# Kernel optimization log

Measured on AMD Instinct MI355X. Metric: run time of the kernel, lower is better.

## Reference

```python
import math
import jax, jax.numpy as jnp
import numpy as np
from jax.scipy.special import gammaln, xlogy

B, N1, N2 = 4, 2048, 512
D, H, DK = 768, 8, 64
DV = D // H        # 96 (dim_value = dim // heads)
NRP = D // H       # 96 num_rel_pos_features (divisible by 6)
DY0 = 1280 + 256   # esm_dim + cell_line_dim
EPS = 1e-5
SCALE = DK ** -0.5


def layer_norm(z, g, b):
    m = jnp.mean(z, -1, keepdims=True)
    v = jnp.mean(jnp.square(z - m), -1, keepdims=True)
    return (z - m) * jax.lax.rsqrt(v + EPS) * g + b


def get_positional_embed(seq_len, feature_size):
    # Enformer-style relative positional features over distances [-(L-1), L-1]
    d = jnp.arange(-seq_len + 1, seq_len)
    ad = jnp.abs(d).astype(jnp.float32)[:, None]  # [2L-1, 1]
    nb = feature_size // 6
    # exponential half-life basis
    max_range = math.log(seq_len) / math.log(2.0)
    half_life = 2.0 ** jnp.linspace(3.0, max_range, nb)
    f_exp = jnp.exp(-math.log(2.0) / half_life * ad)
    # central mask basis
    cw = 2.0 ** jnp.arange(1, nb + 1).astype(jnp.float32) - 1.0
    f_cm = (cw > ad).astype(jnp.float32)
    # gamma pdf basis
    stddev = seq_len / (2.0 * nb)
    start_mean = seq_len / nb
    mean = jnp.linspace(start_mean, float(seq_len), nb)
    conc = (mean / stddev) ** 2
    rate = mean / (stddev ** 2)
    logp = xlogy(conc - 1.0, ad) - rate * ad - (gammaln(conc) - conc * jnp.log(rate))
    prob = jnp.exp(logp) + 1e-8
    f_g = prob / jnp.max(prob, -1, keepdims=True)
    emb = jnp.concatenate([f_exp, f_cm, f_g], -1)  # [2L-1, feature_size/2]
    sign = jnp.sign(d).astype(jnp.float32)[:, None]
    return jnp.concatenate([emb, sign * emb], -1)  # [2L-1, feature_size]


def relative_shift(z):
    # Transformer-XL shift: [b,h,i,2*L-1] -> [b,h,i,L]
    b, h, i, j = z.shape
    z = jnp.pad(z, ((0, 0), (0, 0), (0, 0), (1, 0)))
    z = z.reshape(b, h, j + 1, i)[:, :, 1:, :].reshape(b, h, i, j)
    return z[..., : (j + 2) // 2]


def ffn(z, g, b, w1, b1, w2, b2):
    h = layer_norm(z, g, b)
    h = jax.nn.relu(h @ w1 + b1)
    return z + h @ w2 + b2


def setup_inputs() -> dict:
    key = jax.random.key(0)
    ks = jax.random.split(key, 32)
    p = lambda i, shape, s=0.02: jax.random.normal(ks[i], shape, jnp.float32) * s
    return dict(
        x=jax.random.normal(ks[0], (B, N1, D), jnp.float32),
        y0=jax.random.normal(ks[1], (B, N2, DY0), jnp.float32),
        W_res=p(2, (DY0, D)),
        lnx_g=jnp.ones((D,)), lnx_b=jnp.zeros((D,)),
        lny_g=jnp.ones((D,)), lny_b=jnp.zeros((D,)),
        Wq=p(3, (D, H * DK)), Wk=p(4, (D, H * DK)),
        Wv1=p(5, (D, H * DV)), Wv2=p(6, (D, H * DV)),
        Wo1=p(7, (H * DV, D)), bo1=jnp.zeros((D,)),
        Wo2=p(8, (H * DV, D)), bo2=jnp.zeros((D,)),
        Wrel=p(9, (NRP, H * DK)),
        rel_pos_bias=p(10, (H, DK), 1.0),
        fx_g=jnp.ones((D,)), fx_b=jnp.zeros((D,)),
        fx_w1=p(11, (D, 2 * D)), fx_b1=jnp.zeros((2 * D,)),
        fx_w2=p(12, (2 * D, D)), fx_b2=jnp.zeros((D,)),
        fy_g=jnp.ones((D,)), fy_b=jnp.zeros((D,)),
        fy_w1=p(13, (D, 2 * D)), fy_b1=jnp.zeros((2 * D,)),
        fy_w2=p(14, (2 * D, D)), fy_b2=jnp.zeros((D,)),
    )


def reference(x, y0, W_res, lnx_g, lnx_b, lny_g, lny_b, Wq, Wk, Wv1, Wv2,
              Wo1, bo1, Wo2, bo2, Wrel, rel_pos_bias,
              fx_g, fx_b, fx_w1, fx_b1, fx_w2, fx_b2,
              fy_g, fy_b, fy_w1, fy_b1, fy_w2, fy_b2):
    b, n1, _ = x.shape
    n2 = y0.shape[1]
    y = y0 @ W_res                               # res_proj (first layer)
    x1 = layer_norm(x, lnx_g, lnx_b)
    y1 = layer_norm(y, lny_g, lny_b)

    q = (x1 @ Wq).reshape(b, n1, H, DK).transpose(0, 2, 1, 3) * SCALE
    k = (y1 @ Wk).reshape(b, n2, H, DK).transpose(0, 2, 1, 3)
    v2 = (y1 @ Wv2).reshape(b, n2, H, DV).transpose(0, 2, 1, 3)

    content = jnp.einsum('bhid,bhjd->bhij', q, k)  # [b,h,n1,n2]

    pos = get_positional_embed(n1, NRP)            # [2*n1-1, NRP]
    rel_q = (pos @ Wrel).reshape(2 * n1 - 1, H, DK).transpose(1, 0, 2)
    kb = k * SCALE + rel_pos_bias[None, :, None, :]
    rel = jnp.einsum('bhjd,hmd->bhjm', kb, rel_q)  # [b,h,n2,2*n1-1]
    rel = relative_shift(rel)                      # [b,h,n2,n1]
    logits = content + rel.transpose(0, 1, 3, 2)

    attn = jax.nn.softmax(logits, -1)
    out1 = jnp.einsum('bhij,bhjd->bhid', attn, v2)
    out1 = out1.transpose(0, 2, 1, 3).reshape(b, n1, H * DV)
    x2 = out1 @ Wo1 + bo1

    v1 = (x1 @ Wv1).reshape(b, n1, H, DV).transpose(0, 2, 1, 3)
    out2 = jnp.einsum('bhij,bhid->bhjd', attn, v1)  # attn^T @ v1
    out2 = out2.transpose(0, 2, 1, 3).reshape(b, n2, H * DV)
    y2 = out2 @ Wo2 + bo2

    x4 = x + x2
    x5 = ffn(x4, fx_g, fx_b, fx_w1, fx_b1, fx_w2, fx_b2)
    y4 = y2 + y
    y5 = ffn(y4, fy_g, fy_b, fy_w1, fy_b1, fy_w2, fy_b2)
    return (x5, y5)
```

## Files before the change

kernel.cpp:

```cpp
#include <hip/hip_runtime.h>
#include <hip/hip_bf16.h>
#include <math.h>

typedef __hip_bfloat16 bf16;
typedef short s16x8 __attribute__((ext_vector_type(8)));
typedef short s16x4 __attribute__((ext_vector_type(4)));
typedef float f32x4 __attribute__((ext_vector_type(4)));

#define B_    4
#define N1_   2048
#define N2_   512
#define D_    768
#define H_    8
#define DK_   64
#define DV_   96
#define NPOS_ 4095
#define SCALE_ 0.125f

__device__ __forceinline__ float b2f(bf16 v) { return __bfloat162float(v); }
__device__ __forceinline__ bf16  f2b(float v) { return __float2bfloat16(v); }
__device__ __forceinline__ float us2f(unsigned short u) {
    return __uint_as_float(((unsigned int)u) << 16);
}
__device__ __forceinline__ unsigned short f2bu(float v) {
    bf16 t = __float2bfloat16(v);
    return *reinterpret_cast<unsigned short*>(&t);
}
__device__ __forceinline__ float ldf(const float* p) { return *p; }
__device__ __forceinline__ float ldf(const bf16* p)  { return __bfloat162float(*p); }
__device__ __forceinline__ void stf(float* p, float v) { *p = v; }
__device__ __forceinline__ void stf(bf16* p, float v)  { *p = f2b(v); }
#define MFMA16(a, b, c) __builtin_amdgcn_mfma_f32_16x16x32_bf16((a), (b), (c), 0, 0, 0)

__device__ __forceinline__ void gl16(const unsigned short* g, unsigned short* l) {
    __builtin_amdgcn_global_load_lds(
        (const __attribute__((address_space(1))) unsigned int*)g,
        (__attribute__((address_space(3))) unsigned int*)l, 16, 0, 0);
}

struct PackT {
    const float* src[12];
    unsigned K[12], N[12], dbase[12], drow[12];
    unsigned t0[13];
};

__global__ __launch_bounds__(256) void packT_kernel(PackT pa, bf16* __restrict__ dst)
{
    int bid = blockIdx.x, s = 0;
    while (s < 11 && bid >= (int)pa.t0[s + 1]) s++;
    int t = bid - (int)pa.t0[s];
    unsigned K = pa.K[s], N = pa.N[s];
    unsigned ntk = K >> 5;
    unsigned k0 = (t % ntk) << 5, n0 = (t / ntk) << 6;
    __shared__ float tile[32][65];
    const float* src = pa.src[s];
    int tid = threadIdx.x;
    {
        int e = tid * 8, k = e >> 6, n = e & 63;
        const float* p = src + (size_t)(k0 + k) * N + n0 + n;
#pragma unroll
        for (int j = 0; j < 8; j++) tile[k][n + j] = p[j];
    }
    __syncthreads();
    {
        int f = tid * 8, n = f >> 5, k = f & 31;
        bf16* q = dst + (size_t)pa.dbase[s] + (size_t)(n0 + n) * pa.drow[s] + k0 + k;
#pragma unroll
        for (int j = 0; j < 8; j++) q[j] = f2b(tile[k + j][n]);
    }
}

template <typename T>
__global__ __launch_bounds__(64) void lnfull_kernel(
    const T* __restrict__ in, const float* __restrict__ g,
    const float* __restrict__ b, bf16* __restrict__ out)
{
    int row = blockIdx.x, lane = threadIdx.x;
    const T* p = in + (size_t)row * D_;
    float v[12];
    float s = 0.f;
#pragma unroll
    for (int i = 0; i < 12; i++) { v[i] = ldf(p + lane + i * 64); s += v[i]; }
#pragma unroll
    for (int o = 32; o > 0; o >>= 1) s += __shfl_down(s, o);
    float mean = __shfl(s, 0) * (1.f / 768.f);
    float var = 0.f;
#pragma unroll
    for (int i = 0; i < 12; i++) { float d = v[i] - mean; var += d * d; }
#pragma unroll
    for (int o = 32; o > 0; o >>= 1) var += __shfl_down(var, o);
    float rstd = rsqrtf(__shfl(var, 0) * (1.f / 768.f) + 1e-5f);
    bf16* q = out + (size_t)row * D_;
#pragma unroll
    for (int i = 0; i < 12; i++) {
        int c = lane + i * 64;
        q[c] = f2b((v[i] - mean) * rstd * g[c] + b[c]);
    }
}

template <int AM, typename TC, typename TR>
__device__ __forceinline__ void gemm128_body(
    unsigned short* As, unsigned short* Bs, int tid,
    const void* Av, const bf16* BwT, TC* C, int M, int N, int K,
    const float* bias, int relu, const TR* res,
    bf16* Cq, bf16* Cv, bf16* Cq2, const float* qbias2,
    float sscale, int vshift, int bm, int bn)
{
    int wave = tid >> 6, lane = tid & 63;
    int lc = lane & 15, kq = lane >> 4;
    int wm = (wave & 1) * 64, wn = (wave >> 1) * 64;
    f32x4 acc[4][4] = {};
    int grow = tid >> 3, gcol = (tid & 7) * 8;
    const unsigned short* bg = (const unsigned short*)BwT + (size_t)(bn + grow) * K + gcol;
    unsigned short* asl = As + wave * 512;
    unsigned short* bsl = Bs + wave * 512;
    const size_t SL = (size_t)B_ * N2_ * 768;

    for (int k0 = 0; k0 < K; k0 += 64) {
        if (AM == 0) {
            const unsigned short* ag = (const unsigned short*)Av + (size_t)(bm + grow) * K + k0 + gcol;
#pragma unroll
            for (int it = 0; it < 4; it++)
                gl16(ag + (size_t)(it * 32) * K, asl + it * 2048);
        } else {
#pragma unroll
            for (int it = 0; it < 4; it++) {
                const unsigned short* a0 = (const unsigned short*)Av
                    + (size_t)(bm + grow + it * 32) * K + k0 + gcol;
                s16x8 v0 = *reinterpret_cast<const s16x8*>(a0);
                s16x8 v1 = *reinterpret_cast<const s16x8*>(a0 + SL);
                s16x8 v2 = *reinterpret_cast<const s16x8*>(a0 + 2 * SL);
                s16x8 v3 = *reinterpret_cast<const s16x8*>(a0 + 3 * SL);
                s16x8 w;
#pragma unroll
                for (int j = 0; j < 8; j++)
                    w[j] = (short)f2bu(us2f((unsigned short)v0[j]) + us2f((unsigned short)v1[j]) +
                                       us2f((unsigned short)v2[j]) + us2f((unsigned short)v3[j]));
                *reinterpret_cast<s16x8*>(&As[(grow + it * 32) * 64 + gcol]) = w;
            }
        }
#pragma unroll
        for (int it = 0; it < 4; it++)
            gl16(bg + (size_t)(it * 32) * K + k0, bsl + it * 2048);
        __syncthreads();
#pragma unroll
        for (int kh = 0; kh < 2; kh++) {
            s16x8 af[4], bf[4];
#pragma unroll
            for (int mt = 0; mt < 4; mt++)
                af[mt] = *reinterpret_cast<const s16x8*>(&As[(wm + mt * 16 + lc) * 64 + kh * 32 + kq * 8]);
#pragma unroll
            for (int nt = 0; nt < 4; nt++)
                bf[nt] = *reinterpret_cast<const s16x8*>(&Bs[(wn + nt * 16 + lc) * 64 + kh * 32 + kq * 8]);
#pragma unroll
            for (int mt = 0; mt < 4; mt++)
#pragma unroll
                for (int nt = 0; nt < 4; nt++)
                    acc[mt][nt] = MFMA16(af[mt], bf[nt], acc[mt][nt]);
        }
        __syncthreads();
    }

#pragma unroll
    for (int mt = 0; mt < 4; mt++) {
#pragma unroll
        for (int nt = 0; nt < 4; nt++) {
            int n = bn + wn + nt * 16 + lc;
            float bv = (!Cq && bias) ? bias[n] : 0.f;
#pragma unroll
            for (int r = 0; r < 4; r++) {
                int m = bm + wm + mt * 16 + kq * 4 + r;
                float vr = acc[mt][nt][r];
                if (Cq) {
                    int rows = 1 << vshift;
                    int bb = m >> vshift, rr = m & (rows - 1);
                    if (n < 512) {
                        size_t off = (((size_t)bb * 8 + (n >> 6)) * rows + rr) * 64 + (n & 63);
                        Cq[off] = f2b(vr * sscale);
                        if (Cq2) Cq2[off] = f2b(vr * SCALE_ + qbias2[n]);
                    } else {
                        int nn = n - 512, hh = nn / 96, dv = nn - hh * 96;
                        Cv[(((size_t)bb * 8 + hh) * rows + rr) * 96 + dv] = f2b(vr);
                    }
                } else {
                    float v = vr + bv;
                    if (relu) v = fmaxf(v, 0.f);
                    size_t off = (size_t)m * N + n;
                    if (res) v += ldf(res + off);
                    stf(C + off, v);
                }
            }
        }
    }
}

struct GP {
    const void* Av; const bf16* BwT; void* C;
    int M, N, K;
    const float* bias; int relu; const void* res;
    bf16 *Cq, *Cv, *Cq2; const float* qbias2;
    float sscale; int vshift; int nbx, nwg;
};

template <int AMA, int AMB, typename TC, typename TR>
__global__ __launch_bounds__(256, 4) void dual128_kernel(GP a, GP b)
{
    __shared__ __align__(16) unsigned short As[128 * 64];
    __shared__ __align__(16) unsigned short Bs[128 * 64];
    int tid = threadIdx.x;
    int bid = blockIdx.x;
    if (bid < a.nwg) {
        int sbid = (a.nwg & 7) ? bid : ((bid & 7) * (a.nwg >> 3) + (bid >> 3));
        gemm128_body<AMA, TC, TR>(As, Bs, tid, a.Av, a.BwT, (TC*)a.C,
            a.M, a.N, a.K, a.bias, a.relu, (const TR*)a.res,
            a.Cq, a.Cv, a.Cq2, a.qbias2, a.sscale, a.vshift,
            (sbid / a.nbx) * 128, (sbid % a.nbx) * 128);
    } else {
        int lb = bid - a.nwg;
        int sbid = (b.nwg & 7) ? lb : ((lb & 7) * (b.nwg >> 3) + (lb >> 3));
        gemm128_body<AMB, TC, TR>(As, Bs, tid, b.Av, b.BwT, (TC*)b.C,
            b.M, b.N, b.K, b.bias, b.relu, (const TR*)b.res,
            b.Cq, b.Cv, b.Cq2, b.qbias2, b.sscale, b.vshift,
            (sbid / b.nbx) * 128, (sbid % b.nbx) * 128);
    }
}

template <int AM, typename TC>
__global__ __launch_bounds__(256) void mgemm64_kernel(
    const void* __restrict__ Av, const bf16* __restrict__ BwT,
    TC* __restrict__ C, int M, int N, int K)
{
    __shared__ unsigned short As[64][40];
    __shared__ unsigned short Bs[64][40];
    int tid = threadIdx.x, wave = tid >> 6, lane = tid & 63;
    int bm = blockIdx.y * 64, bn = blockIdx.x * 64;
    f32x4 acc[4] = {};
    int am = tid >> 2, ak = (tid & 3) * 8;
    int bn_ = tid & 63, bk = (tid >> 6) * 8;
    const unsigned short* bwt = (const unsigned short*)BwT;

    for (int k0 = 0; k0 < K; k0 += 32) {
        if (AM == 0) {
            s16x8 va = {};
            if (bm + am < M)
                va = *reinterpret_cast<const s16x8*>(
                    (const unsigned short*)Av + (size_t)(bm + am) * K + k0 + ak);
            *reinterpret_cast<s16x8*>(&As[am][ak]) = va;
        } else {
            const float* ap = (const float*)Av + (size_t)(bm + am) * K + k0 + ak;
#pragma unroll
            for (int j = 0; j < 8; j++)
                As[am][ak + j] = (bm + am < M) ? f2bu(ap[j]) : (unsigned short)0;
        }
        *reinterpret_cast<s16x8*>(&Bs[bn_][bk]) =
            *reinterpret_cast<const s16x8*>(bwt + (size_t)(bn + bn_) * K + k0 + bk);
        __syncthreads();

        s16x8 afrag = *reinterpret_cast<const s16x8*>(&As[wave * 16 + (lane & 15)][(lane >> 4) * 8]);
#pragma unroll
        for (int ns = 0; ns < 4; ns++) {
            s16x8 bfrag = *reinterpret_cast<const s16x8*>(&Bs[ns * 16 + (lane & 15)][(lane >> 4) * 8]);
            acc[ns] = MFMA16(afrag, bfrag, acc[ns]);
        }
        __syncthreads();
    }

    int col = lane & 15, rg = (lane >> 4) * 4;
#pragma unroll
    for (int ns = 0; ns < 4; ns++) {
        int n = bn + ns * 16 + col;
#pragma unroll
        for (int r = 0; r < 4; r++) {
            int m = bm + wave * 16 + rg + r;
            if (m >= M) continue;
            stf(C + (size_t)m * N + n, acc[ns][r]);
        }
    }
}

__global__ __launch_bounds__(64) void pos_kernel(bf16* __restrict__ pos)
{
    int m = blockIdx.x * 64 + threadIdx.x;
    if (m >= NPOS_) return;
    float dist = (float)(m - 2047);
    float ad = fabsf(dist);
    float sgn = (dist > 0.f) ? 1.f : ((dist < 0.f) ? -1.f : 0.f);
    float f[48];
#pragma unroll
    for (int t = 0; t < 16; t++) {
        float hl = exp2f(3.f + (8.f / 15.f) * (float)t);
        f[t] = expf(-0.69314718056f / hl * ad);
    }
#pragma unroll
    for (int t = 0; t < 16; t++) {
        float cw = exp2f((float)(t + 1)) - 1.f;
        f[16 + t] = (cw > ad) ? 1.f : 0.f;
    }
    float pr[16];
    float mx = 0.f;
    if (ad < 0.5f) {
#pragma unroll
        for (int t = 0; t < 16; t++) pr[t] = 1e-8f;
        mx = 1e-8f;
    } else {
        float lad = logf(ad);
#pragma unroll
        for (int t = 0; t < 16; t++) {
            float mean = 128.f * (float)(t + 1);
            float cc = (mean / 64.f) * (mean / 64.f);
            float rate = mean * (1.f / 4096.f);
            float logp = (cc - 1.f) * lad - rate * ad - (lgammaf(cc) - cc * logf(rate));
            float p = expf(logp) + 1e-8f;
            pr[t] = p;
            mx = fmaxf(mx, p);
        }
    }
#pragma unroll
    for (int t = 0; t < 16; t++) f[32 + t] = pr[t] / mx;

    bf16* o = pos + (size_t)m * 96;
#pragma unroll
    for (int c = 0; c < 48; c++) { o[c] = f2b(f[c]); o[48 + c] = f2b(sgn * f[c]); }
}

#define TP_ 344
__global__ __launch_bounds__(256) void tshift_kernel(
    const bf16* __restrict__ kbb, const bf16* __restrict__ relq,
    bf16* __restrict__ tsh, int base, int plen)
{
    int mc = blockIdx.x, jt = blockIdx.y, bh = blockIdx.z;
    int mbase = mc << 8, jg0 = jt << 6, h = bh & 7;
    int iwin0 = mbase + jg0 - 511 - base;
    if (iwin0 + 318 < 0 || iwin0 >= plen) return;
    int a0 = iwin0 & 7;
    int iwa = iwin0 - a0;
    __shared__ unsigned short Tl[64][TP_];
    int tid = threadIdx.x, wave = tid >> 6, lane = tid & 63;
    int lc = lane & 15, kq = lane >> 4;

    const bf16* ap = kbb + ((size_t)bh * N2_ + jg0 + wave * 16 + lc) * 64 + kq * 8;
    s16x8 af0 = *reinterpret_cast<const s16x8*>(ap);
    s16x8 af1 = *reinterpret_cast<const s16x8*>(ap + 32);

    int jrow = wave * 16 + kq * 4;
#pragma unroll
    for (int sub = 0; sub < 2; sub++) {
        int m0 = mbase + sub * 128;
        f32x4 tacc[8] = {};
#pragma unroll
        for (int ns = 0; ns < 8; ns++) {
            const bf16* rp = relq + (size_t)(m0 + ns * 16 + lc) * 512 + h * 64 + kq * 8;
            s16x8 rf0 = *reinterpret_cast<const s16x8*>(rp);
            s16x8 rf1 = *reinterpret_cast<const s16x8*>(rp + 32);
            tacc[ns] = MFMA16(af0, rf0, tacc[ns]);
            tacc[ns] = MFMA16(af1, rf1, tacc[ns]);
        }
#pragma unroll
        for (int ns = 0; ns < 8; ns++)
#pragma unroll
            for (int r = 0; r < 4; r++) {
                int col = sub * 128 + ns * 16 + lc + jrow + r + a0;
                Tl[jrow + r][col] = f2bu(tacc[ns][r]);
            }
    }
    __syncthreads();

    int row = tid >> 2, q = tid & 3;
    int cstart = row + a0;
    bf16* out = tsh + ((size_t)bh * N2_ + jg0 + row) * (size_t)plen;
#pragma unroll
    for (int s = 0; s < 11; s++) {
        int c = (q + s * 4) * 8;
        int i = iwa + c;
        if (c >= cstart && c + 8 <= cstart + 256 && i >= 0 && i + 8 <= plen) {
            *reinterpret_cast<s16x8*>(out + i) =
                *reinterpret_cast<const s16x8*>(&Tl[row][c]);
        } else {
#pragma unroll
            for (int e = 0; e < 8; e++) {
                int ce = c + e, ie = i + e;
                if (ce >= cstart && ce < cstart + 256 && ie >= 0 && ie < plen)
                    out[ie] = *reinterpret_cast<const bf16*>(&Tl[row][ce]);
            }
        }
    }
}

__global__ __launch_bounds__(256) void attn1_kernel(
    const bf16* __restrict__ qb, const bf16* __restrict__ kb,
    const bf16* __restrict__ tsh, const bf16* __restrict__ v2,
    bf16* __restrict__ out1, float* __restrict__ mst, float* __restrict__ lst,
    int base, int tpitch)
{
    int bh = blockIdx.y;
    int b = bh >> 3, h = bh & 7;
    int i0 = base + blockIdx.x * 64;
    __shared__ __align__(16) unsigned short Ts[64][72];
    __shared__ __align__(16) unsigned short Ps[64][72];
    __shared__ __align__(16) unsigned short Vs[96][72];
    int tid = threadIdx.x, wave = tid >> 6, lane = tid & 63;
    int lc = lane & 15, kq = lane >> 4;
    int ibase = wave * 16 + kq * 4;

    const bf16* qp = qb + ((size_t)bh * N1_ + i0 + wave * 16 + lc) * 64 + kq * 8;
    s16x8 qf0 = *reinterpret_cast<const s16x8*>(qp);
    s16x8 qf1 = *reinterpret_cast<const s16x8*>(qp + 32);

    int trow = tid >> 2, tchunk = tid & 3;
    const unsigned short* tb0 = (const unsigned short*)tsh
        + ((size_t)bh * N2_ + trow) * tpitch + (i0 - base) + tchunk * 16;
    const unsigned short* vb0 = (const unsigned short*)v2
        + ((size_t)bh * N2_ + trow) * 96 + tchunk * 24;

    float m_run[4], l_run[4];
#pragma unroll
    for (int r = 0; r < 4; r++) { m_run[r] = -1e30f; l_run[r] = 0.f; }
    f32x4 oacc[6] = {};

    for (int j0 = 0; j0 < N2_; j0 += 64) {
        __syncthreads();
        {
            const unsigned short* p = tb0 + (size_t)j0 * tpitch;
            *reinterpret_cast<s16x8*>(&Ts[trow][tchunk * 16]) =
                *reinterpret_cast<const s16x8*>(p);
            *reinterpret_cast<s16x8*>(&Ts[trow][tchunk * 16 + 8]) =
                *reinterpret_cast<const s16x8*>(p + 8);
        }
        {
            const unsigned short* p = vb0 + (size_t)j0 * 96;
            s16x8 w0 = *reinterpret_cast<const s16x8*>(p);
            s16x8 w1 = *reinterpret_cast<const s16x8*>(p + 8);
            s16x8 w2 = *reinterpret_cast<const s16x8*>(p + 16);
            int vd = tchunk * 24;
#pragma unroll
            for (int s = 0; s < 8; s++) Vs[vd + s][trow] = (unsigned short)w0[s];
#pragma unroll
            for (int s = 0; s < 8; s++) Vs[vd + 8 + s][trow] = (unsigned short)w1[s];
#pragma unroll
            for (int s = 0; s < 8; s++) Vs[vd + 16 + s][trow] = (unsigned short)w2[s];
        }
        __syncthreads();

        f32x4 cacc[4] = {};
#pragma unroll
        for (int ns = 0; ns < 4; ns++) {
            const bf16* kp = kb + ((size_t)bh * N2_ + j0 + ns * 16 + lc) * 64 + kq * 8;
            s16x8 kf0 = *reinterpret_cast<const s16x8*>(kp);
            s16x8 kf1 = *reinterpret_cast<const s16x8*>(kp + 32);
            cacc[ns] = MFMA16(qf0, kf0, cacc[ns]);
            cacc[ns] = MFMA16(qf1, kf1, cacc[ns]);
        }
        float Lv[4][4];
#pragma unroll
        for (int ns = 0; ns < 4; ns++) {
            int jloc = ns * 16 + lc;
            s16x4 tv = *reinterpret_cast<const s16x4*>(&Ts[jloc][ibase]);
#pragma unroll
            for (int r = 0; r < 4; r++)
                Lv[ns][r] = cacc[ns][r] + us2f((unsigned short)tv[r]);
        }
#pragma unroll
        for (int r = 0; r < 4; r++) {
            float v = fmaxf(fmaxf(Lv[0][r], Lv[1][r]), fmaxf(Lv[2][r], Lv[3][r]));
            v = fmaxf(v, __shfl_xor(v, 1));
            v = fmaxf(v, __shfl_xor(v, 2));
            v = fmaxf(v, __shfl_xor(v, 4));
            v = fmaxf(v, __shfl_xor(v, 8));
            float mn = fmaxf(m_run[r], v);
            float alpha = __expf(m_run[r] - mn);
            m_run[r] = mn;
            float s = 0.f;
#pragma unroll
            for (int ns = 0; ns < 4; ns++) {
                float p = __expf(Lv[ns][r] - mn);
                Lv[ns][r] = p;
                s += p;
            }
            s += __shfl_xor(s, 1);
            s += __shfl_xor(s, 2);
            s += __shfl_xor(s, 4);
            s += __shfl_xor(s, 8);
            l_run[r] = l_run[r] * alpha + s;
#pragma unroll
            for (int ns6 = 0; ns6 < 6; ns6++) oacc[ns6][r] *= alpha;
        }
#pragma unroll
        for (int ns = 0; ns < 4; ns++)
#pragma unroll
            for (int r = 0; r < 4; r++)
                Ps[ibase + r][ns * 16 + lc] = f2bu(Lv[ns][r]);
#pragma unroll
        for (int kk = 0; kk < 2; kk++) {
            s16x8 pf = *reinterpret_cast<const s16x8*>(&Ps[wave * 16 + lc][kq * 8 + kk * 32]);
#pragma unroll
            for (int ns6 = 0; ns6 < 6; ns6++) {
                s16x8 vf = *reinterpret_cast<const s16x8*>(&Vs[ns6 * 16 + lc][kq * 8 + kk * 32]);
                oacc[ns6] = MFMA16(pf, vf, oacc[ns6]);
            }
        }
    }

    float invl[4];
#pragma unroll
    for (int r = 0; r < 4; r++) invl[r] = 1.f / l_run[r];
#pragma unroll
    for (int ns6 = 0; ns6 < 6; ns6++)
#pragma unroll
        for (int r = 0; r < 4; r++)
            out1[(size_t)(b * N1_ + i0 + ibase + r) * 768 + h * 96 + ns6 * 16 + lc]
                = f2b(oacc[ns6][r] * invl[r]);
    if (lc == 0) {
#pragma unroll
        for (int r = 0; r < 4; r++) {
            mst[(size_t)bh * N1_ + i0 + ibase + r] = m_run[r];
            lst[(size_t)bh * N1_ + i0 + ibase + r] = l_run[r];
        }
    }
}

__global__ __launch_bounds__(256) void attn2_kernel(
    const bf16* __restrict__ qb, const bf16* __restrict__ kb,
    const bf16* __restrict__ tsh, const bf16* __restrict__ v1,
    bf16* __restrict__ out2b, const float* __restrict__ mst,
    const float* __restrict__ lst, int base, int tpitch)
{
    int jt = blockIdx.x, bh = blockIdx.y;
    int b = bh >> 3, h = bh & 7;
    int ib = base + blockIdx.z * 512;
    bf16* out2 = out2b + (size_t)(ib >> 9) * ((size_t)B_ * N2_ * 768);
    int j0 = jt * 64;
    __shared__ __align__(16) unsigned short Ts[64][72];
    __shared__ __align__(16) unsigned short Ps[64][72];
    __shared__ __align__(16) unsigned short Vs[96][72];
    int tid = threadIdx.x, wave = tid >> 6, lane = tid & 63;
    int lc = lane & 15, kq = lane >> 4;
    int ibase = wave * 16 + kq * 4;

    s16x8 kf0[4], kf1[4];
#pragma unroll
    for (int ns = 0; ns < 4; ns++) {
        const bf16* kp = kb + ((size_t)bh * N2_ + j0 + ns * 16 + lc) * 64 + kq * 8;
        kf0[ns] = *reinterpret_cast<const s16x8*>(kp);
        kf1[ns] = *reinterpret_cast<const s16x8*>(kp + 32);
    }

    int trow = tid >> 2, tchunk = tid & 3;
    const unsigned short* tb0 = (const unsigned short*)tsh
        + ((size_t)bh * N2_ + j0 + trow) * tpitch + tchunk * 16;
    const unsigned short* vb0 = (const unsigned short*)v1
        + ((size_t)bh * N1_ + trow) * 96 + tchunk * 24;

    f32x4 oacc[6] = {};
    for (int i0 = ib; i0 < ib + 512; i0 += 64) {
        __syncthreads();
        {
            const unsigned short* p = tb0 + (i0 - base);
            *reinterpret_cast<s16x8*>(&Ts[trow][tchunk * 16]) =
                *reinterpret_cast<const s16x8*>(p);
            *reinterpret_cast<s16x8*>(&Ts[trow][tchunk * 16 + 8]) =
                *reinterpret_cast<const s16x8*>(p + 8);
        }
        {
            const unsigned short* p = vb0 + (size_t)i0 * 96;
            s16x8 w0 = *reinterpret_cast<const s16x8*>(p);
            s16x8 w1 = *reinterpret_cast<const s16x8*>(p + 8);
            s16x8 w2 = *reinterpret_cast<const s16x8*>(p + 16);
            int vd = tchunk * 24;
#pragma unroll
            for (int s = 0; s < 8; s++) Vs[vd + s][trow] = (unsigned short)w0[s];
#pragma unroll
            for (int s = 0; s < 8; s++) Vs[vd + 8 + s][trow] = (unsigned short)w1[s];
#pragma unroll
            for (int s = 0; s < 8; s++) Vs[vd + 16 + s][trow] = (unsigned short)w2[s];
        }
        __syncthreads();

        const bf16* qp = qb + ((size_t)bh * N1_ + i0 + wave * 16 + lc) * 64 + kq * 8;
        s16x8 qf0 = *reinterpret_cast<const s16x8*>(qp);
        s16x8 qf1 = *reinterpret_cast<const s16x8*>(qp + 32);
        f32x4 cacc[4] = {};
#pragma unroll
        for (int ns = 0; ns < 4; ns++) {
            cacc[ns] = MFMA16(qf0, kf0[ns], cacc[ns]);
            cacc[ns] = MFMA16(qf1, kf1[ns], cacc[ns]);
        }
        float mi[4], invli[4];
#pragma unroll
        for (int r = 0; r < 4; r++) {
            mi[r] = mst[(size_t)bh * N1_ + i0 + ibase + r];
            invli[r] = 1.f / lst[(size_t)bh * N1_ + i0 + ibase + r];
        }
#pragma unroll
        for (int ns = 0; ns < 4; ns++) {
            int jloc = ns * 16 + lc;
            s16x4 tv = *reinterpret_cast<const s16x4*>(&Ts[jloc][ibase]);
            s16x4 pw;
#pragma unroll
            for (int r = 0; r < 4; r++) {
                float L = cacc[ns][r] + us2f((unsigned short)tv[r]);
                pw[r] = (short)f2bu(__expf(L - mi[r]) * invli[r]);
            }
            *reinterpret_cast<s16x4*>(&Ps[jloc][ibase]) = pw;
        }
        __syncthreads();
#pragma unroll
        for (int kk = 0; kk < 2; kk++) {
            s16x8 pf = *reinterpret_cast<const s16x8*>(&Ps[wave * 16 + lc][kq * 8 + kk * 32]);
#pragma unroll
            for (int ns6 = 0; ns6 < 6; ns6++) {
                s16x8 vf = *reinterpret_cast<const s16x8*>(&Vs[ns6 * 16 + lc][kq * 8 + kk * 32]);
                oacc[ns6] = MFMA16(pf, vf, oacc[ns6]);
            }
        }
    }

#pragma unroll
    for (int ns6 = 0; ns6 < 6; ns6++)
#pragma unroll
        for (int r = 0; r < 4; r++)
            out2[(size_t)(b * N2_ + j0 + ibase + r) * 768 + h * 96 + ns6 * 16 + lc]
                = f2b(oacc[ns6][r]);
}

extern "C" void kernel_launch(void* const* d_in, const int* in_sizes, int n_in,
                              void* d_out, int out_size, void* d_ws, size_t ws_size,
                              hipStream_t stream)
{
    (void)in_sizes; (void)n_in; (void)out_size;
    const float* x      = (const float*)d_in[0];
    const float* y0     = (const float*)d_in[1];
    const float* Wres   = (const float*)d_in[2];
    const float* lnx_g  = (const float*)d_in[3];
    const float* lnx_b  = (const float*)d_in[4];
    const float* lny_g  = (const float*)d_in[5];
    const float* lny_b  = (const float*)d_in[6];
    const float* Wq     = (const float*)d_in[7];
    const float* Wk     = (const float*)d_in[8];
    const float* Wv1    = (const float*)d_in[9];
    const float* Wv2    = (const float*)d_in[10];
    const float* Wo1    = (const float*)d_in[11];
    const float* bo1    = (const float*)d_in[12];
    const float* Wo2    = (const float*)d_in[13];
    const float* bo2    = (const float*)d_in[14];
    const float* Wrel   = (const float*)d_in[15];
    const float* rel_pb = (const float*)d_in[16];
    const float* fx_g   = (const float*)d_in[17];
    const float* fx_b   = (const float*)d_in[18];
    const float* fx_w1  = (const float*)d_in[19];
    const float* fx_b1  = (const float*)d_in[20];
    const float* fx_w2  = (const float*)d_in[21];
    const float* fx_b2  = (const float*)d_in[22];
    const float* fy_g   = (const float*)d_in[23];
    const float* fy_b   = (const float*)d_in[24];
    const float* fy_w1  = (const float*)d_in[25];
    const float* fy_b1  = (const float*)d_in[26];
    const float* fy_w2  = (const float*)d_in[27];
    const float* fy_b2  = (const float*)d_in[28];

    float* out_x = (float*)d_out;
    float* out_y = out_x + (size_t)B_ * N1_ * D_;
    bf16* out1 = (bf16*)d_out;

    char* W = (char*)d_ws;
    size_t o = 0;
    auto alloc = [&](size_t bytes) { char* p = W + o; o += (bytes + 255) & ~(size_t)255; return p; };
    bf16*   qb   = (bf16*)alloc((size_t)B_ * N1_ * 512 * 2);
    bf16*   kb   = (bf16*)alloc((size_t)B_ * N2_ * 512 * 2);
    bf16*   posb = (bf16*)alloc((size_t)NPOS_ * 96 * 2);
    bf16*   relq = (bf16*)alloc((size_t)NPOS_ * 512 * 2);
    bf16*   v1b  = (bf16*)alloc((size_t)B_ * N1_ * 768 * 2);
    bf16*   hx2  = (bf16*)alloc((size_t)B_ * N1_ * 768 * 2);
    bf16*   v2b  = (bf16*)alloc((size_t)B_ * N2_ * 768 * 2);
    float*  yb   = (float*)alloc((size_t)B_ * N2_ * 768 * 4);
    bf16*   kbbb = (bf16*)alloc((size_t)B_ * N2_ * 512 * 2);
    bf16*   wpool= (bf16*)alloc((size_t)9093120 * 2);
    float*  mst  = (float*)alloc((size_t)B_ * H_ * N1_ * 4);
    float*  lst  = (float*)alloc((size_t)B_ * H_ * N1_ * 4);

    size_t x1y1 = ((size_t)B_ * N1_ * 768 + (size_t)B_ * N2_ * 768) * 2;
    size_t rem = ws_size > o ? ws_size - o : 0;
    int plen = 512;
    if (rem >= (size_t)32 * 512 * 2048 * 2 + 1024) plen = 2048;
    else if (rem >= (size_t)32 * 512 * 1024 * 2 + 1024) plen = 1024;
    size_t tshB = (size_t)32 * 512 * (size_t)plen * 2;
    bf16* tshb = (bf16*)alloc(tshB > x1y1 ? tshB : x1y1);
    bf16* x1 = tshb;
    bf16* y1 = x1 + (size_t)B_ * N1_ * 768;

    bf16* x4 = qb;
    bf16* y4 = v2b;
    bf16* hx = v1b;
    bf16* out2h = hx2;
    bf16* hy = (bf16*)yb;
    bf16* x4ln = x1;
    bf16* y4ln = y1;

    const unsigned OW_RES = 0, OW_QV1 = 1179648, OW_KV2 = 2162688, OW_O1 = 3145728,
                   OW_O2 = 3735552, OW_REL = 4325376, OW_FXW1 = 4374528,
                   OW_FXW2 = 5554176, OW_FYW1 = 6733824, OW_FYW2 = 7913472;

    PackT pa;
    const float* srcs[12] = {Wres, Wq, Wv1, Wk, Wv2, Wo1, Wo2, Wrel,
                             fx_w1, fx_w2, fy_w1, fy_w2};
    unsigned Ks[12] = {1536, 768, 768, 768, 768, 768, 768, 96, 768, 1536, 768, 1536};
    unsigned Nss[12] = {768, 512, 768, 512, 768, 768, 768, 512, 1536, 768, 1536, 768};
    unsigned dbs[12] = {OW_RES, OW_QV1, OW_QV1 + 393216, OW_KV2, OW_KV2 + 393216,
                        OW_O1, OW_O2, OW_REL, OW_FXW1, OW_FXW2, OW_FYW1, OW_FYW2};
    unsigned drs[12] = {1536, 768, 768, 768, 768, 768, 768, 96, 768, 1536, 768, 1536};
    unsigned cum = 0;
    for (int i = 0; i < 12; i++) {
        pa.src[i] = srcs[i]; pa.K[i] = Ks[i]; pa.N[i] = Nss[i];
        pa.dbase[i] = dbs[i]; pa.drow[i] = drs[i];
        pa.t0[i] = cum;
        cum += (Ks[i] >> 5) * (Nss[i] >> 6);
    }
    pa.t0[12] = cum;

    dim3 blk(256);
    packT_kernel<<<cum, blk, 0, stream>>>(pa, wpool);
    mgemm64_kernel<1, float><<<dim3(12, 32), blk, 0, stream>>>(
        y0, wpool + OW_RES, yb, B_ * N2_, D_, 1536);
    lnfull_kernel<float><<<B_ * N1_, 64, 0, stream>>>(x, lnx_g, lnx_b, x1);
    lnfull_kernel<float><<<B_ * N2_, 64, 0, stream>>>(yb, lny_g, lny_b, y1);
    {
        GP a{x1, wpool + OW_QV1, nullptr, B_ * N1_, 1280, D_,
             nullptr, 0, nullptr, qb, v1b, nullptr, nullptr, SCALE_, 11, 10, 640};
        GP b{y1, wpool + OW_KV2, nullptr, B_ * N2_, 1280, D_,
             nullptr, 0, nullptr, kb, v2b, kbbb, rel_pb, 1.f, 9, 10, 160};
        dual128_kernel<0, 0, bf16, float><<<800, blk, 0, stream>>>(a, b);
    }
    pos_kernel<<<(NPOS_ + 63) / 64, 64, 0, stream>>>(posb);
    mgemm64_kernel<0, bf16><<<dim3(8, 64), blk, 0, stream>>>(
        posb, wpool + OW_REL, relq, NPOS_, 512, 96);
    for (int base = 0; base < N1_; base += plen) {
        tshift_kernel<<<dim3(10, 8, 32), blk, 0, stream>>>(kbbb, relq, tshb, base, plen);
        attn1_kernel<<<dim3(plen / 64, 32), blk, 0, stream>>>(
            qb, kb, tshb, v2b, out1, mst, lst, base, plen);
        attn2_kernel<<<dim3(8, 32, plen / 512), blk, 0, stream>>>(
            qb, kb, tshb, v1b, out2h, mst, lst, base, plen);
    }
    {
        GP a{out1, wpool + OW_O1, x4, B_ * N1_, D_, D_,
             bo1, 0, x, nullptr, nullptr, nullptr, nullptr, 0.f, 0, 6, 384};
        GP b{out2h, wpool + OW_O2, y4, B_ * N2_, D_, D_,
             bo2, 0, yb, nullptr, nullptr, nullptr, nullptr, 0.f, 0, 6, 96};
        dual128_kernel<0, 2, bf16, float><<<480, blk, 0, stream>>>(a, b);
    }
    lnfull_kernel<bf16><<<B_ * N1_, 64, 0, stream>>>(x4, fx_g, fx_b, x4ln);
    lnfull_kernel<bf16><<<B_ * N2_, 64, 0, stream>>>(y4, fy_g, fy_b, y4ln);
    {
        GP a{x4ln, wpool + OW_FXW1, hx, B_ * N1_, 1536, D_,
             fx_b1, 1, nullptr, nullptr, nullptr, nullptr, nullptr, 0.f, 0, 12, 768};
        GP b{y4ln, wpool + OW_FYW1, hy, B_ * N2_, 1536, D_,
             fy_b1, 1, nullptr, nullptr, nullptr, nullptr, nullptr, 0.f, 0, 12, 192};
        dual128_kernel<0, 0, bf16, float><<<960, blk, 0, stream>>>(a, b);
    }
    {
        GP a{hx, wpool + OW_FXW2, out_x, B_ * N1_, D_, 1536,
             fx_b2, 0, x4, nullptr, nullptr, nullptr, nullptr, 0.f, 0, 6, 384};
        GP b{hy, wpool + OW_FYW2, out_y, B_ * N2_, D_, 1536,
             fy_b2, 0, y4, nullptr, nullptr, nullptr, nullptr, 0.f, 0, 6, 96};
        dual128_kernel<0, 0, float, bf16><<<480, blk, 0, stream>>>(a, b);
    }
}
```

Baseline: 600.4 us.

## Split-K the y0 residual GEMM and fold rel-pos GEMM into QKV launch

The fp32-input 64x64 residual GEMM on y0 is replaced by an fp32-to-bf16 conversion pass, a 4-way split-K 128x128 MFMA GEMM writing partials, and a fused reduce+LayerNorm kernel that produces both yb and y1. The small pos@Wrel GEMM is appended as extra workgroups to the dual QKV GEMM launch, so it no longer needs its own launch. This targets low parallelism and slow per-element conversion in the old small-tile kernel, and also removes launch gaps. The cost is extra global traffic for the partial sums and the converted copy.

```diff
diff --git a/kernel.cpp b/kernel.cpp
--- a/kernel.cpp
+++ b/kernel.cpp
@@ -70,6 +70,21 @@
     }
 }
 
+__global__ __launch_bounds__(256) void cvt8_kernel(
+    const float* __restrict__ in, bf16* __restrict__ out)
+{
+    int i = (blockIdx.x * 256 + threadIdx.x) * 8;
+    f32x4 a = *reinterpret_cast<const f32x4*>(in + i);
+    f32x4 b = *reinterpret_cast<const f32x4*>(in + i + 4);
+    s16x8 w;
+#pragma unroll
+    for (int j = 0; j < 4; j++) {
+        w[j] = (short)f2bu(a[j]);
+        w[4 + j] = (short)f2bu(b[j]);
+    }
+    *reinterpret_cast<s16x8*>((unsigned short*)out + i) = w;
+}
+
 template <typename T>
 __global__ __launch_bounds__(64) void lnfull_kernel(
     const T* __restrict__ in, const float* __restrict__ g,
@@ -91,6 +106,101 @@
     for (int o = 32; o > 0; o >>= 1) var += __shfl_down(var, o);
     float rstd = rsqrtf(__shfl(var, 0) * (1.f / 768.f) + 1e-5f);
     bf16* q = out + (size_t)row * D_;
+#pragma unroll
+    for (int i = 0; i < 12; i++) {
+        int c = lane + i * 64;
+        q[c] = f2b((v[i] - mean) * rstd * g[c] + b[c]);
+    }
+}
+
+__global__ __launch_bounds__(256, 4) void wres_splitk_kernel(
+    const bf16* __restrict__ Av, const bf16* __restrict__ BwT,
+    float* __restrict__ Cp)
+{
+    __shared__ __align__(16) unsigned short As[128 * 64];
+    __shared__ __align__(16) unsigned short Bs[128 * 64];
+    const int K = 1536;
+    int tid = threadIdx.x, wave = tid >> 6, lane = tid & 63;
+    int lc = lane & 15, kq = lane >> 4;
+    int wm = (wave & 1) * 64, wn = (wave >> 1) * 64;
+    int bid = blockIdx.x;
+    int sbid = (bid & 7) * 48 + (bid >> 3);
+    int s = sbid / 96, t = sbid % 96;
+    int bm = (t / 6) * 128, bn = (t % 6) * 128;
+    int ks = s * 384;
+    f32x4 acc[4][4] = {};
+    int grow = tid >> 3, gcol = (tid & 7) * 8;
+    const unsigned short* ag = (const unsigned short*)Av + (size_t)(bm + grow) * K + gcol;
+    const unsigned short* bg = (const unsigned short*)BwT + (size_t)(bn + grow) * K + gcol;
+    unsigned short* asl = As + wave * 512;
+    unsigned short* bsl = Bs + wave * 512;
+
+    for (int k0 = ks; k0 < ks + 384; k0 += 64) {
+#pragma unroll
+        for (int it = 0; it < 4; it++) {
+            gl16(ag + (size_t)(it * 32) * K + k0, asl + it * 2048);
+            gl16(bg + (size_t)(it * 32) * K + k0, bsl + it * 2048);
+        }
+        __syncthreads();
+#pragma unroll
+        for (int kh = 0; kh < 2; kh++) {
+            s16x8 af[4], bf[4];
+#pragma unroll
+            for (int mt = 0; mt < 4; mt++)
+                af[mt] = *reinterpret_cast<const s16x8*>(&As[(wm + mt * 16 + lc) * 64 + kh * 32 + kq * 8]);
+#pragma unroll
+            for (int nt = 0; nt < 4; nt++)
+                bf[nt] = *reinterpret_cast<const s16x8*>(&Bs[(wn + nt * 16 + lc) * 64 + kh * 32 + kq * 8]);
+#pragma unroll
+            for (int mt = 0; mt < 4; mt++)
+#pragma unroll
+                for (int nt = 0; nt < 4; nt++)
+                    acc[mt][nt] = MFMA16(af[mt], bf[nt], acc[mt][nt]);
+        }
+        __syncthreads();
+    }
+
+    float* out = Cp + (size_t)s * (2048 * 768);
+#pragma unroll
+    for (int mt = 0; mt < 4; mt++)
+#pragma unroll
+        for (int nt = 0; nt < 4; nt++) {
+            int n = bn + wn + nt * 16 + lc;
+#pragma unroll
+            for (int r = 0; r < 4; r++) {
+                int m = bm + wm + mt * 16 + kq * 4 + r;
+                out[(size_t)m * 768 + n] = acc[mt][nt][r];
+            }
+        }
+}
+
+__global__ __launch_bounds__(64) void lnred4_kernel(
+    const float* __restrict__ Cp, const float* __restrict__ g,
+    const float* __restrict__ b, float* __restrict__ yb, bf16* __restrict__ y1)
+{
+    int row = blockIdx.x, lane = threadIdx.x;
+    const size_t SL = (size_t)2048 * 768;
+    const float* p = Cp + (size_t)row * 768;
+    float* yo = yb + (size_t)row * 768;
+    float v[12];
+    float s = 0.f;
+#pragma unroll
+    for (int i = 0; i < 12; i++) {
+        int c = lane + i * 64;
+        float t = p[c] + p[SL + c] + p[2 * SL + c] + p[3 * SL + c];
+        v[i] = t; s += t;
+        yo[c] = t;
+    }
+#pragma unroll
+    for (int o = 32; o > 0; o >>= 1) s += __shfl_down(s, o);
+    float mean = __shfl(s, 0) * (1.f / 768.f);
+    float var = 0.f;
+#pragma unroll
+    for (int i = 0; i < 12; i++) { float d = v[i] - mean; var += d * d; }
+#pragma unroll
+    for (int o = 32; o > 0; o >>= 1) var += __shfl_down(var, o);
+    float rstd = rsqrtf(__shfl(var, 0) * (1.f / 768.f) + 1e-5f);
+    bf16* q = y1 + (size_t)row * D_;
 #pragma unroll
     for (int i = 0; i < 12; i++) {
         int c = lane + i * 64;
@@ -225,55 +335,65 @@
     }
 }
 
-template <int AM, typename TC>
-__global__ __launch_bounds__(256) void mgemm64_kernel(
-    const void* __restrict__ Av, const bf16* __restrict__ BwT,
-    TC* __restrict__ C, int M, int N, int K)
-{
-    __shared__ unsigned short As[64][40];
-    __shared__ unsigned short Bs[64][40];
-    int tid = threadIdx.x, wave = tid >> 6, lane = tid & 63;
-    int bm = blockIdx.y * 64, bn = blockIdx.x * 64;
-    f32x4 acc[4] = {};
-    int am = tid >> 2, ak = (tid & 3) * 8;
-    int bn_ = tid & 63, bk = (tid >> 6) * 8;
-    const unsigned short* bwt = (const unsigned short*)BwT;
-
-    for (int k0 = 0; k0 < K; k0 += 32) {
-        if (AM == 0) {
+__global__ __launch_bounds__(256, 4) void dual3_kernel(GP a, GP b,
+    const bf16* __restrict__ relA, const bf16* __restrict__ relB,
+    bf16* __restrict__ relC)
+{
+    __shared__ __align__(16) unsigned short As[128 * 64];
+    __shared__ __align__(16) unsigned short Bs[128 * 64];
+    int tid = threadIdx.x;
+    int bid = blockIdx.x;
+    if (bid < a.nwg) {
+        int sbid = (bid & 7) * (a.nwg >> 3) + (bid >> 3);
+        gemm128_body<0, bf16, float>(As, Bs, tid, a.Av, a.BwT, (bf16*)a.C,
+            a.M, a.N, a.K, a.bias, a.relu, (const float*)a.res,
+            a.Cq, a.Cv, a.Cq2, a.qbias2, a.sscale, a.vshift,
+            (sbid / a.nbx) * 128, (sbid % a.nbx) * 128);
+    } else if (bid < a.nwg + b.nwg) {
+        int lb = bid - a.nwg;
+        int sbid = (lb & 7) * (b.nwg >> 3) + (lb >> 3);
+        gemm128_body<0, bf16, float>(As, Bs, tid, b.Av, b.BwT, (bf16*)b.C,
+            b.M, b.N, b.K, b.bias, b.relu, (const float*)b.res,
+            b.Cq, b.Cv, b.Cq2, b.qbias2, b.sscale, b.vshift,
+            (sbid / b.nbx) * 128, (sbid % b.nbx) * 128);
+    } else {
+        int lb = bid - a.nwg - b.nwg;
+        int slb = (lb & 7) * 64 + (lb >> 3);
+        int bm = (slb >> 3) * 64, bn = (slb & 7) * 64;
+        const int M = NPOS_, N = 512, K = 96;
+        unsigned short (*A6)[40] = (unsigned short (*)[40])As;
+        unsigned short (*B6)[40] = (unsigned short (*)[40])Bs;
+        int wave = tid >> 6, lane = tid & 63;
+        f32x4 acc[4] = {};
+        int am = tid >> 2, ak = (tid & 3) * 8;
+        int bn_ = tid & 63, bk = (tid >> 6) * 8;
+        for (int k0 = 0; k0 < K; k0 += 32) {
             s16x8 va = {};
             if (bm + am < M)
                 va = *reinterpret_cast<const s16x8*>(
-                    (const unsigned short*)Av + (size_t)(bm + am) * K + k0 + ak);
-            *reinterpret_cast<s16x8*>(&As[am][ak]) = va;
-        } else {
-            const float* ap = (const float*)Av + (size_t)(bm + am) * K + k0 + ak;
-#pragma unroll
-            for (int j = 0; j < 8; j++)
-                As[am][ak + j] = (bm + am < M) ? f2bu(ap[j]) : (unsigned short)0;
-        }
-        *reinterpret_cast<s16x8*>(&Bs[bn_][bk]) =
-            *reinterpret_cast<const s16x8*>(bwt + (size_t)(bn + bn_) * K + k0 + bk);
-        __syncthreads();
-
-        s16x8 afrag = *reinterpret_cast<const s16x8*>(&As[wave * 16 + (lane & 15)][(lane >> 4) * 8]);
+                    (const unsigned short*)relA + (size_t)(bm + am) * K + k0 + ak);
+            *reinterpret_cast<s16x8*>(&A6[am][ak]) = va;
+            *reinterpret_cast<s16x8*>(&B6[bn_][bk]) =
+                *reinterpret_cast<const s16x8*>(
+                    (const unsigned short*)relB + (size_t)(bn + bn_) * K + k0 + bk);
+            __syncthreads();
+            s16x8 af = *reinterpret_cast<const s16x8*>(&A6[wave * 16 + (lane & 15)][(lane >> 4) * 8]);
+#pragma unroll
+            for (int ns = 0; ns < 4; ns++) {
+                s16x8 bf = *reinterpret_cast<const s16x8*>(&B6[ns * 16 + (lane & 15)][(lane >> 4) * 8]);
+                acc[ns] = MFMA16(af, bf, acc[ns]);
+            }
+            __syncthreads();
+        }
+        int col = lane & 15, rg = (lane >> 4) * 4;
 #pragma unroll
         for (int ns = 0; ns < 4; ns++) {
-            s16x8 bfrag = *reinterpret_cast<const s16x8*>(&Bs[ns * 16 + (lane & 15)][(lane >> 4) * 8]);
-            acc[ns] = MFMA16(afrag, bfrag, acc[ns]);
-        }
-        __syncthreads();
-    }
-
-    int col = lane & 15, rg = (lane >> 4) * 4;
-#pragma unroll
-    for (int ns = 0; ns < 4; ns++) {
-        int n = bn + ns * 16 + col;
-#pragma unroll
-        for (int r = 0; r < 4; r++) {
-            int m = bm + wave * 16 + rg + r;
-            if (m >= M) continue;
-            stf(C + (size_t)m * N + n, acc[ns][r]);
+            int n = bn + ns * 16 + col;
+#pragma unroll
+            for (int r = 0; r < 4; r++) {
+                int m = bm + wave * 16 + rg + r;
+                if (m < M) relC[(size_t)m * N + n] = f2b(acc[ns][r]);
+            }
         }
     }
 }
@@ -687,6 +807,8 @@
     bf16* x1 = tshb;
     bf16* y1 = x1 + (size_t)B_ * N1_ * 768;
 
+    bf16* y0b = qb;
+    float* Cp = (float*)v1b;
     bf16* x4 = qb;
     bf16* y4 = v2b;
     bf16* hx = v1b;
@@ -718,20 +840,18 @@
 
     dim3 blk(256);
     packT_kernel<<<cum, blk, 0, stream>>>(pa, wpool);
-    mgemm64_kernel<1, float><<<dim3(12, 32), blk, 0, stream>>>(
-        y0, wpool + OW_RES, yb, B_ * N2_, D_, 1536);
+    cvt8_kernel<<<(B_ * N2_ * 1536) / 2048, blk, 0, stream>>>(y0, y0b);
+    pos_kernel<<<(NPOS_ + 63) / 64, 64, 0, stream>>>(posb);
     lnfull_kernel<float><<<B_ * N1_, 64, 0, stream>>>(x, lnx_g, lnx_b, x1);
-    lnfull_kernel<float><<<B_ * N2_, 64, 0, stream>>>(yb, lny_g, lny_b, y1);
+    wres_splitk_kernel<<<384, blk, 0, stream>>>(y0b, wpool + OW_RES, Cp);
+    lnred4_kernel<<<B_ * N2_, 64, 0, stream>>>(Cp, lny_g, lny_b, yb, y1);
     {
         GP a{x1, wpool + OW_QV1, nullptr, B_ * N1_, 1280, D_,
              nullptr, 0, nullptr, qb, v1b, nullptr, nullptr, SCALE_, 11, 10, 640};
         GP b{y1, wpool + OW_KV2, nullptr, B_ * N2_, 1280, D_,
              nullptr, 0, nullptr, kb, v2b, kbbb, rel_pb, 1.f, 9, 10, 160};
-        dual128_kernel<0, 0, bf16, float><<<800, blk, 0, stream>>>(a, b);
-    }
-    pos_kernel<<<(NPOS_ + 63) / 64, 64, 0, stream>>>(posb);
-    mgemm64_kernel<0, bf16><<<dim3(8, 64), blk, 0, stream>>>(
-        posb, wpool + OW_REL, relq, NPOS_, 512, 96);
+        dual3_kernel<<<1312, blk, 0, stream>>>(a, b, posb, wpool + OW_REL, relq);
+    }
     for (int base = 0; base < N1_; base += plen) {
         tshift_kernel<<<dim3(10, 8, 32), blk, 0, stream>>>(kbbb, relq, tshb, base, plen);
         attn1_kernel<<<dim3(plen / 64, 32), blk, 0, stream>>>(
```

After: 556.4 us. 7.3% less time.
